# Optimization experiments

Measured on AMD Instinct MI355X. Metric: run time of the kernel, lower is better.

Reference implementation:

```python
import jax, jax.numpy as jnp
import numpy as np

# dims (match init_kwargs)
B, T, F = 2048, 252, 64      # batch, n_timestep, n_feature
C, L, K = 64, 4, 3           # channels, num levels, kernel_size
NOUT, NSEL = 500, 20         # n_output assets, n_select
LB, UB = 0.0, 0.1            # simplex box bounds
N_REBAL_ITERS = 16           # fixed bound on the water-filling loop (converges in a few iters)


def setup_inputs() -> dict:
    key = jax.random.key(0)
    ks = jax.random.split(key, 12)
    inp = {
        'x': jax.random.normal(ks[0], (B, T, F), dtype=jnp.float32),
        # TemporalBlock convs: init_weights() uses N(0, 0.01); weight_norm is a
        # reparametrization, so the effective conv weight is just a dense tensor.
        'conv1_w': 0.01 * jax.random.normal(ks[1], (L, C, C, K), dtype=jnp.float32),
        'conv1_b': 0.01 * jax.random.normal(ks[2], (L, C), dtype=jnp.float32),
        'conv2_w': 0.01 * jax.random.normal(ks[3], (L, C, C, K), dtype=jnp.float32),
        'conv2_b': 0.01 * jax.random.normal(ks[4], (L, C), dtype=jnp.float32),
        'proj_w': 0.05 * jax.random.normal(ks[5], (C, C), dtype=jnp.float32),
        'proj_b': 0.01 * jax.random.normal(ks[6], (C,), dtype=jnp.float32),
        'attn_w': 0.05 * jax.random.normal(ks[7], (NOUT, C), dtype=jnp.float32),
        'attn_b': 0.01 * jax.random.normal(ks[8], (NOUT,), dtype=jnp.float32),
        'fc_w': 0.05 * jax.random.normal(ks[9], (NOUT, C), dtype=jnp.float32),
        'fc_b': 0.01 * jax.random.normal(ks[10], (NOUT,), dtype=jnp.float32),
    }
    return inp


def _causal_conv(h, w, b, dil):
    # h: [B,C,T], w: [O,I,K]. torch pads both sides by (K-1)*dil then Chomp1d
    # removes the right pad -> equivalent to pure left (causal) padding.
    k = w.shape[-1]
    out = jax.lax.conv_general_dilated(
        h, w, window_strides=(1,), padding=[((k - 1) * dil, 0)],
        rhs_dilation=(dil,), dimension_numbers=('NCH', 'OIH', 'NCH'))
    return out + b[None, :, None]


def _rebalance(w, lb, ub, n_iters=N_REBAL_ITERS):
    # batched water-filling on the box-bounded simplex; mirrors the torch
    # do-while: redistribute clamped-off mass proportionally to non-capped weights.
    def step(old, wc):
        leftover = jnp.sum(old - wc)
        m = wc != ub
        nsum = jnp.sum(jnp.where(m, wc, 0.0))
        nsum = jnp.where(nsum == 0.0, 1.0, nsum)  # guard degenerate all-capped case
        return jnp.where(m, wc + leftover * wc / nsum, wc)

    cur = step(w, jnp.clip(w, lb, ub))           # first iteration (do-while)
    done0 = ~jnp.any(cur > ub)

    def body(carry, _):
        cur, done = carry
        nxt = step(cur, jnp.clip(cur, lb, ub))
        new = jnp.where(done, cur, nxt)
        return (new, done | ~jnp.any(new > ub)), None

    (res, _), _ = jax.lax.scan(body, (cur, done0), None, length=n_iters)
    return res


def reference(x, conv1_w, conv1_b, conv2_w, conv2_b,
              proj_w, proj_b, attn_w, attn_b, fc_w, fc_b):
    h = jnp.transpose(x, (0, 2, 1))  # [B,F,T]
    for i in range(L):  # fixed small loop over levels (structurally distinct dilations)
        d = 2 ** i
        o = jax.nn.relu(_causal_conv(h, conv1_w[i], conv1_b[i], d))
        o = jax.nn.relu(_causal_conv(o, conv2_w[i], conv2_b[i], d))
        h = jax.nn.relu(o + h)  # in==out channels -> identity residual
    pooled = jnp.max(h, axis=2)                       # MaxPool1d(T) + squeeze -> [B,C]
    z = jax.nn.relu(pooled @ proj_w.T + proj_b)       # proj (dropout=eval no-op)
    attn = jax.nn.sigmoid(z @ attn_w.T + attn_b)      # [B,NOUT]
    _, idx = jax.lax.top_k(attn, NSEL)
    mask = jnp.zeros_like(attn).at[jnp.arange(attn.shape[0])[:, None], idx].set(1.0)
    out = jax.nn.softmax(z @ fc_w.T + fc_b, axis=1) * mask
    out = out / (jnp.sum(out, axis=1, keepdims=True) + 1e-8)
    out = jax.vmap(lambda w: _rebalance(w, LB, UB))(out)
    return out
```

## Files before the change

kernel.cpp:

```cpp
#include <hip/hip_runtime.h>
#include <hip/hip_bf16.h>

#define T 252
#define NOUT 500
#define NSEL 20
#define UBV 0.1f

#define ROWS 272
#define PLANE_U (ROWS * 32)
#define LDS_BYTES (2 * PLANE_U * 4)

#define OFF_AWT    98304
#define OFF_FWT    130304
#define OFF_POOLED 162304

typedef short bf8 __attribute__((ext_vector_type(8)));
typedef float f32x4 __attribute__((ext_vector_type(4)));

static __device__ __forceinline__ unsigned short f2bf(float f) {
    unsigned u = __float_as_uint(f);
    return (unsigned short)((u + 0x7fffu + ((u >> 16) & 1u)) >> 16);
}
static __device__ __forceinline__ float bf2f(unsigned short h) {
    return __uint_as_float(((unsigned)h) << 16);
}
static __device__ __forceinline__ unsigned pk2bf(float a, float b) {
    __hip_bfloat162 h = __float22bfloat162_rn(float2{a, b});
    unsigned u; __builtin_memcpy(&u, &h, 4); return u;
}
static __device__ __forceinline__ float bf_lo_f(unsigned u) { return __uint_as_float(u << 16); }
static __device__ __forceinline__ float bf_hi_f(unsigned u) { return __uint_as_float(u & 0xffff0000u); }
static __device__ __forceinline__ int swz(int row, int chunk) {
    return row * 32 + ((chunk ^ (row & 7)) << 2);
}

__global__ __launch_bounds__(256) void prep_kernel(
    const float* __restrict__ w1, const float* __restrict__ w2,
    const float* __restrict__ aw, const float* __restrict__ fw,
    float* __restrict__ ws)
{
    int gid = blockIdx.x * 256 + threadIdx.x;
    if (gid < 24576) {
        int frag = gid >> 6, lane = gid & 63;
        int s   = frag & 1;
        int m   = (frag >> 1) & 3;
        int t3  = frag >> 3;
        int tap = t3 % 3;
        int q   = t3 / 3;
        int Kt  = q & 1;
        int lvl = (q >> 1) & 3;
        int buf = q >> 3;
        int c  = m * 16 + (lane & 15);
        int i0 = Kt * 32 + (lane >> 4) * 8;
        const float* W = (buf ? w2 : w1) + lvl * 12288 + c * 192;
        unsigned short v[8];
        for (int j = 0; j < 8; ++j) {
            float x = W[(i0 + j) * 3 + tap];
            unsigned short hi = f2bf(x);
            if (s == 0) v[j] = hi;
            else        v[j] = f2bf(x - bf2f(hi));
        }
        unsigned* dst = (unsigned*)ws + frag * 256 + lane * 4;
        for (int d = 0; d < 4; ++d)
            dst[d] = (unsigned)v[2 * d] | ((unsigned)v[2 * d + 1] << 16);
    }
    if (gid < 32000) {
        int a = gid >> 6, c = gid & 63;
        ws[OFF_AWT + c * 500 + a] = aw[gid];
        ws[OFF_FWT + c * 500 + a] = fw[gid];
    }
}

extern __shared__ unsigned short lds[];

#define MFMA(A, B, C) __builtin_amdgcn_mfma_f32_16x16x32_bf16((A), (B), (C), 0, 0, 0)

static __device__ __forceinline__ void conv_mm(
    const uint4* __restrict__ AF4,
    const unsigned* __restrict__ Lh, const unsigned* __restrict__ Ll,
    const float* __restrict__ bias,
    int cvlvl, int d, int Rb, int g, int g4, int lane,
    f32x4 acc[4][4])
{
    #pragma unroll
    for (int m = 0; m < 4; ++m) {
        float4 bv = *(const float4*)(bias + m * 16 + g4);
        #pragma unroll
        for (int nn = 0; nn < 4; ++nn)
            acc[m][nn] = (f32x4){bv.x, bv.y, bv.z, bv.w};
    }
    #pragma unroll
    for (int Kt = 0; Kt < 2; ++Kt) {
        #pragma unroll
        for (int tap = 0; tap < 3; ++tap) {
            const int fb = ((cvlvl * 2 + Kt) * 3 + tap) * 8;
            const uint4* af = AF4 + fb * 64 + lane;
            uint4 ta[4], tb[4];
            #pragma unroll
            for (int m = 0; m < 4; ++m) { ta[m] = af[m * 128]; tb[m] = af[m * 128 + 64]; }
            const int shift = (2 - tap) * d;
            const int row0  = Rb - shift;
            const int ui0   = row0 * 32 + ((((Kt << 2) + g) ^ (row0 & 7)) << 2);
            bf8 Bh[4], Bl[4];
            #pragma unroll
            for (int nn = 0; nn < 4; ++nn) {
                Bh[nn] = *(const bf8*)(Lh + ui0 + nn * 512);
                Bl[nn] = *(const bf8*)(Ll + ui0 + nn * 512);
            }
            #pragma unroll
            for (int m = 0; m < 4; ++m) {
                bf8 Ah = *(bf8*)&ta[m];
                bf8 Al = *(bf8*)&tb[m];
                #pragma unroll
                for (int nn = 0; nn < 4; ++nn) {
                    f32x4 a = acc[m][nn];
                    a = MFMA(Ah, Bh[nn], a);
                    a = MFMA(Ah, Bl[nn], a);
                    a = MFMA(Al, Bh[nn], a);
                    acc[m][nn] = a;
                }
            }
        }
    }
}

__global__ __launch_bounds__(256, 2) void conv_kernel(
    const float* __restrict__ x,
    const float* __restrict__ ws,
    const float* __restrict__ b1,
    const float* __restrict__ b2,
    float* __restrict__ pooled)
{
    const int b    = blockIdx.x;
    const int tid  = threadIdx.x;
    const int lane = tid & 63;
    const int wv   = tid >> 6;

    unsigned* Lh = (unsigned*)lds;
    unsigned* Ll = Lh + PLANE_U;

    for (int j = tid; j < 640; j += 256) {
        int r20 = j >> 5, col = j & 31;
        int r = (r20 < 16) ? r20 : (252 + r20);
        Lh[r * 32 + col] = 0u;
        Ll[r * 32 + col] = 0u;
    }
    const float4* xb = (const float4*)(x + (size_t)b * (T * 64));
    for (int v = tid; v < T * 16; v += 256) {
        float4 xv = xb[v];
        int t = v >> 4, f4 = v & 15;
        unsigned h01 = pk2bf(xv.x, xv.y);
        unsigned h23 = pk2bf(xv.z, xv.w);
        unsigned l01 = pk2bf(xv.x - bf_lo_f(h01), xv.y - bf_hi_f(h01));
        unsigned l23 = pk2bf(xv.z - bf_lo_f(h23), xv.w - bf_hi_f(h23));
        int row = 16 + t;
        int ui = swz(row, f4 >> 1) + ((f4 & 1) << 1);
        Lh[ui]     = h01;
        Lh[ui + 1] = h23;
        Ll[ui]     = l01;
        Ll[ui + 1] = l23;
    }

    const int g    = lane >> 4;
    const int g4   = g << 2;
    const int ln16 = lane & 15;
    const int Rb   = 16 + 64 * wv + ln16;

    float hr[4][4][4];
    #pragma unroll
    for (int m = 0; m < 4; ++m)
        #pragma unroll
        for (int nn = 0; nn < 4; ++nn) {
            int t = 64 * wv + 16 * nn + ln16;
            if (t < T) {
                float4 v = xb[t * 16 + m * 4 + g];
                hr[m][nn][0] = v.x; hr[m][nn][1] = v.y;
                hr[m][nn][2] = v.z; hr[m][nn][3] = v.w;
            } else {
                hr[m][nn][0] = 0.f; hr[m][nn][1] = 0.f;
                hr[m][nn][2] = 0.f; hr[m][nn][3] = 0.f;
            }
        }
    __syncthreads();

    const uint4* AF4 = (const uint4*)ws;

    int ue[4];
    #pragma unroll
    for (int m = 0; m < 4; ++m)
        ue[m] = Rb * 32 + (((2 * m + (g >> 1)) ^ (Rb & 7)) << 2) + ((g & 1) << 1);

    for (int lvl = 0; lvl < 4; ++lvl) {
        const int d = 1 << lvl;
        f32x4 acc[4][4];

        conv_mm(AF4, Lh, Ll, b1 + lvl * 64, 0 * 4 + lvl, d, Rb, g, g4, lane, acc);
        __syncthreads();
        #pragma unroll
        for (int m = 0; m < 4; ++m)
            #pragma unroll
            for (int nn = 0; nn < 4; ++nn) {
                float o0 = fmaxf(acc[m][nn][0], 0.f);
                float o1 = fmaxf(acc[m][nn][1], 0.f);
                float o2 = fmaxf(acc[m][nn][2], 0.f);
                float o3 = fmaxf(acc[m][nn][3], 0.f);
                uint2 wh, wl;
                wh.x = pk2bf(o0, o1);
                wh.y = pk2bf(o2, o3);
                wl.x = pk2bf(o0 - bf_lo_f(wh.x), o1 - bf_hi_f(wh.x));
                wl.y = pk2bf(o2 - bf_lo_f(wh.y), o3 - bf_hi_f(wh.y));
                int ui = ue[m] + nn * 512;
                *(uint2*)(Lh + ui) = wh;
                *(uint2*)(Ll + ui) = wl;
            }
        __syncthreads();

        conv_mm(AF4, Lh, Ll, b2 + lvl * 64, 1 * 4 + lvl, d, Rb, g, g4, lane, acc);
        #pragma unroll
        for (int m = 0; m < 4; ++m)
            #pragma unroll
            for (int nn = 0; nn < 4; ++nn)
                #pragma unroll
                for (int j = 0; j < 4; ++j)
                    hr[m][nn][j] = fmaxf(fmaxf(acc[m][nn][j], 0.f) + hr[m][nn][j], 0.f);

        if (lvl < 3) {
            __syncthreads();
            #pragma unroll
            for (int m = 0; m < 4; ++m)
                #pragma unroll
                for (int nn = 0; nn < 4; ++nn) {
                    float h0 = hr[m][nn][0], h1 = hr[m][nn][1];
                    float h2 = hr[m][nn][2], h3 = hr[m][nn][3];
                    uint2 wh, wl;
                    wh.x = pk2bf(h0, h1);
                    wh.y = pk2bf(h2, h3);
                    wl.x = pk2bf(h0 - bf_lo_f(wh.x), h1 - bf_hi_f(wh.x));
                    wl.y = pk2bf(h2 - bf_lo_f(wh.y), h3 - bf_hi_f(wh.y));
                    int ui = ue[m] + nn * 512;
                    *(uint2*)(Lh + ui) = wh;
                    *(uint2*)(Ll + ui) = wl;
                }
            __syncthreads();
        }
    }

    __syncthreads();
    {
        const bool t3ok = (64 * wv + 48 + ln16) < T;
        float pm[4][4];
        #pragma unroll
        for (int m = 0; m < 4; ++m)
            #pragma unroll
            for (int j = 0; j < 4; ++j) {
                float p = fmaxf(fmaxf(hr[m][0][j], hr[m][1][j]), hr[m][2][j]);
                if (t3ok) p = fmaxf(p, hr[m][3][j]);
                pm[m][j] = p;
            }
        #pragma unroll
        for (int off = 1; off < 16; off <<= 1)
            #pragma unroll
            for (int m = 0; m < 4; ++m)
                #pragma unroll
                for (int j = 0; j < 4; ++j)
                    pm[m][j] = fmaxf(pm[m][j], __shfl_xor(pm[m][j], off));
        float* fp = (float*)lds;
        if (ln16 == 0) {
            #pragma unroll
            for (int m = 0; m < 4; ++m)
                #pragma unroll
                for (int j = 0; j < 4; ++j)
                    fp[wv * 64 + m * 16 + g4 + j] = pm[m][j];
        }
        __syncthreads();
        if (tid < 64) {
            float mm = fmaxf(fmaxf(fp[tid], fp[tid + 64]),
                             fmaxf(fp[tid + 128], fp[tid + 192]));
            pooled[(size_t)b * 64 + tid] = mm;
        }
    }
}

__global__ __launch_bounds__(256) void head_kernel(
    const float* __restrict__ ws,
    const float* __restrict__ proj_w,
    const float* __restrict__ proj_b,
    const float* __restrict__ attn_b,
    const float* __restrict__ fc_b,
    float* __restrict__ out)
{
    const float* awT    = ws + OFF_AWT;
    const float* fwT    = ws + OFF_FWT;
    const float* pooled = ws + OFF_POOLED;

    __shared__ float z[64];
    __shared__ float att[512];
    __shared__ float pa[512];
    __shared__ int   msk[512];
    __shared__ float rs[4];

    const int b   = blockIdx.x;
    const int tid = threadIdx.x;
    const int wv  = tid >> 6, ln = tid & 63;

    {
        const int outc = tid >> 2, part = tid & 3;
        const float* pw = proj_w + outc * 64 + part * 16;
        const float* pl = pooled + (size_t)b * 64 + part * 16;
        float s = 0.f;
        #pragma unroll
        for (int c = 0; c < 16; ++c) s = fmaf(pw[c], pl[c], s);
        s += __shfl_xor(s, 1);
        s += __shfl_xor(s, 2);
        if (part == 0) z[outc] = fmaxf(s + proj_b[outc], 0.f);
    }
    __syncthreads();

    const int a0  = tid;
    const int a1  = tid + 256;
    const int a1e = (a1 < NOUT) ? a1 : (NOUT - 1);

    float l0 = attn_b[a0], l1 = attn_b[a1e];
    float f0 = fc_b[a0],   f1 = fc_b[a1e];
    #pragma unroll 8
    for (int c = 0; c < 64; ++c) {
        float zc = z[c];
        l0 = fmaf(zc, awT[c * 500 + a0],  l0);
        l1 = fmaf(zc, awT[c * 500 + a1e], l1);
        f0 = fmaf(zc, fwT[c * 500 + a0],  f0);
        f1 = fmaf(zc, fwT[c * 500 + a1e], f1);
    }
    float v0 = 1.f / (1.f + expf(-l0));
    float v1 = (a1 < NOUT) ? 1.f / (1.f + expf(-l1)) : 0.f;
    if (a1 >= NOUT) f1 = -1e30f;
    att[a0] = v0; att[a1] = v1;
    msk[a0] = 0;  msk[a1] = 0;
    __syncthreads();

    int selidx = 0;
    if (wv == 0) {
        float va[8];
        #pragma unroll
        for (int j = 0; j < 8; ++j) {
            int id = j * 64 + ln;
            va[j] = (id < NOUT) ? att[id] : 0.f;
        }
        for (int s = 0; s < NSEL; ++s) {
            float bv = va[0]; int bj = 0;
            #pragma unroll
            for (int j = 1; j < 8; ++j)
                if (va[j] > bv) { bv = va[j]; bj = j; }
            unsigned long long k =
                ((unsigned long long)__float_as_uint(bv) << 32)
                | (unsigned)(0xFFFFFFFFu - (unsigned)(bj * 64 + ln));
            for (int o = 32; o > 0; o >>= 1) {
                unsigned long long other = __shfl_xor(k, o);
                if (other > k) k = other;
            }
            int widx = (int)(0xFFFFFFFFu - (unsigned)(k & 0xFFFFFFFFu));
            if (ln == s) selidx = widx;
            if ((widx & 63) == ln) va[widx >> 6] = 0.f;
            if (ln == 0) msk[widx] = 1;
        }
    }
    __syncthreads();

    float mx = fmaxf(f0, f1);
    for (int o = 32; o > 0; o >>= 1) mx = fmaxf(mx, __shfl_xor(mx, o));
    if (ln == 0) rs[wv] = mx;
    __syncthreads();
    mx = fmaxf(fmaxf(rs[0], rs[1]), fmaxf(rs[2], rs[3]));
    __syncthreads();
    float e0 = expf(f0 - mx);
    float e1 = (a1 < NOUT) ? expf(f1 - mx) : 0.f;
    float sm = e0 + e1;
    for (int o = 32; o > 0; o >>= 1) sm += __shfl_xor(sm, o);
    if (ln == 0) rs[wv] = sm;
    __syncthreads();
    float Z = rs[0] + rs[1] + rs[2] + rs[3];

    float p0 = msk[a0] ? (e0 / Z) : 0.f;
    float p1 = (a1 < NOUT && msk[a1]) ? (e1 / Z) : 0.f;
    pa[a0] = p0; pa[a1] = p1;
    __syncthreads();

    if (wv == 0) {
        float w = (ln < NSEL) ? pa[selidx] : 0.f;
        float S = w;
        for (int o = 32; o > 0; o >>= 1) S += __shfl_xor(S, o);
        w = w / (S + 1e-8f);
        for (int it = 0; it < 17; ++it) {
            float wc = fminf(fmaxf(w, 0.f), UBV);
            float lo = w - wc;
            float ns = (wc != UBV) ? wc : 0.f;
            for (int o = 32; o > 0; o >>= 1) {
                lo += __shfl_xor(lo, o);
                ns += __shfl_xor(ns, o);
            }
            if (ns == 0.f) ns = 1.f;
            w = (wc != UBV) ? wc + lo * wc / ns : wc;
        }
        if (ln < NSEL) out[(size_t)b * NOUT + selidx] = w;
    }
    if (!msk[a0]) out[(size_t)b * NOUT + a0] = 0.f;
    if (a1 < NOUT && !msk[a1]) out[(size_t)b * NOUT + a1] = 0.f;
}

extern "C" void kernel_launch(void* const* d_in, const int* in_sizes, int n_in,
                              void* d_out, int out_size, void* d_ws, size_t ws_size,
                              hipStream_t stream)
{
    const float* x   = (const float*)d_in[0];
    const float* c1w = (const float*)d_in[1];
    const float* c1b = (const float*)d_in[2];
    const float* c2w = (const float*)d_in[3];
    const float* c2b = (const float*)d_in[4];
    const float* pw  = (const float*)d_in[5];
    const float* pb  = (const float*)d_in[6];
    const float* aw  = (const float*)d_in[7];
    const float* ab  = (const float*)d_in[8];
    const float* fw  = (const float*)d_in[9];
    const float* fb  = (const float*)d_in[10];

    float* ws  = (float*)d_ws;
    float* out = (float*)d_out;

    (void)hipFuncSetAttribute((const void*)conv_kernel,
                              hipFuncAttributeMaxDynamicSharedMemorySize,
                              LDS_BYTES);

    prep_kernel<<<128, 256, 0, stream>>>(c1w, c2w, aw, fw, ws);
    conv_kernel<<<2048, 256, LDS_BYTES, stream>>>(x, ws, c1b, c2b, ws + OFF_POOLED);
    head_kernel<<<2048, 256, 0, stream>>>(ws, pw, pb, ab, fb, out);
}
```

Before: 510.7 us.

## Use LDS-only barriers, prefetch first weight fragment, and stagger conv blocks

Replaces __syncthreads with a barrier that waits only on LDS counters, so outstanding global loads can stay in flight across barriers. The first weight fragment and bias for the next conv are prefetched before each barrier, overlapping those global loads with synchronisation. MFMA sections are wrapped in s_setprio, and every other group of 256 blocks sleeps briefly at start to stagger its phase against the co-resident block. The custom barrier depends on the compiler not needing vmcnt at those points, and the sleep adds latency if staggering does not help.

Result: slower. 545.8 us (+6.9%).

```diff
diff --git a/kernel.cpp b/kernel.cpp
--- a/kernel.cpp
+++ b/kernel.cpp
@@ -33,6 +33,12 @@
 static __device__ __forceinline__ int swz(int row, int chunk) {
     return row * 32 + ((chunk ^ (row & 7)) << 2);
 }
+
+#define BAR_LDS() do {                                        \
+    asm volatile("s_waitcnt lgkmcnt(0)" ::: "memory");        \
+    __builtin_amdgcn_s_barrier();                             \
+    asm volatile("" ::: "memory");                            \
+} while (0)
 
 __global__ __launch_bounds__(256) void prep_kernel(
     const float* __restrict__ w1, const float* __restrict__ w2,
@@ -75,16 +81,37 @@
 
 #define MFMA(A, B, C) __builtin_amdgcn_mfma_f32_16x16x32_bf16((A), (B), (C), 0, 0, 0)
 
+struct Frag0 {
+    uint4  ta[4], tb[4];
+    float4 bv[4];
+};
+
+static __device__ __forceinline__ Frag0 pf_frag0(
+    const uint4* __restrict__ AF4, int cvlvl, int lane,
+    const float* __restrict__ bias, int g4)
+{
+    Frag0 f;
+    const int fb = (cvlvl * 2 + 0) * 3 + 0;
+    const uint4* af = AF4 + fb * 8 * 64 + lane;
+    #pragma unroll
+    for (int m = 0; m < 4; ++m) {
+        f.ta[m] = af[m * 128];
+        f.tb[m] = af[m * 128 + 64];
+        f.bv[m] = *(const float4*)(bias + m * 16 + g4);
+    }
+    return f;
+}
+
 static __device__ __forceinline__ void conv_mm(
     const uint4* __restrict__ AF4,
     const unsigned* __restrict__ Lh, const unsigned* __restrict__ Ll,
-    const float* __restrict__ bias,
-    int cvlvl, int d, int Rb, int g, int g4, int lane,
+    const Frag0& f0,
+    int cvlvl, int d, int Rb, int g, int lane,
     f32x4 acc[4][4])
 {
     #pragma unroll
     for (int m = 0; m < 4; ++m) {
-        float4 bv = *(const float4*)(bias + m * 16 + g4);
+        float4 bv = f0.bv[m];
         #pragma unroll
         for (int nn = 0; nn < 4; ++nn)
             acc[m][nn] = (f32x4){bv.x, bv.y, bv.z, bv.w};
@@ -93,11 +120,16 @@
     for (int Kt = 0; Kt < 2; ++Kt) {
         #pragma unroll
         for (int tap = 0; tap < 3; ++tap) {
-            const int fb = ((cvlvl * 2 + Kt) * 3 + tap) * 8;
-            const uint4* af = AF4 + fb * 64 + lane;
             uint4 ta[4], tb[4];
-            #pragma unroll
-            for (int m = 0; m < 4; ++m) { ta[m] = af[m * 128]; tb[m] = af[m * 128 + 64]; }
+            if (Kt == 0 && tap == 0) {
+                #pragma unroll
+                for (int m = 0; m < 4; ++m) { ta[m] = f0.ta[m]; tb[m] = f0.tb[m]; }
+            } else {
+                const int fb = ((cvlvl * 2 + Kt) * 3 + tap) * 8;
+                const uint4* af = AF4 + fb * 64 + lane;
+                #pragma unroll
+                for (int m = 0; m < 4; ++m) { ta[m] = af[m * 128]; tb[m] = af[m * 128 + 64]; }
+            }
             const int shift = (2 - tap) * d;
             const int row0  = Rb - shift;
             const int ui0   = row0 * 32 + ((((Kt << 2) + g) ^ (row0 & 7)) << 2);
@@ -107,6 +139,7 @@
                 Bh[nn] = *(const bf8*)(Lh + ui0 + nn * 512);
                 Bl[nn] = *(const bf8*)(Ll + ui0 + nn * 512);
             }
+            __builtin_amdgcn_s_setprio(1);
             #pragma unroll
             for (int m = 0; m < 4; ++m) {
                 bf8 Ah = *(bf8*)&ta[m];
@@ -120,6 +153,7 @@
                     acc[m][nn] = a;
                 }
             }
+            __builtin_amdgcn_s_setprio(0);
         }
     }
 }
@@ -135,6 +169,8 @@
     const int tid  = threadIdx.x;
     const int lane = tid & 63;
     const int wv   = tid >> 6;
+
+    if ((blockIdx.x >> 8) & 1) __builtin_amdgcn_s_sleep(127);
 
     unsigned* Lh = (unsigned*)lds;
     unsigned* Ll = Lh + PLANE_U;
@@ -181,9 +217,11 @@
                 hr[m][nn][2] = 0.f; hr[m][nn][3] = 0.f;
             }
         }
-    __syncthreads();
 
     const uint4* AF4 = (const uint4*)ws;
+
+    Frag0 f0 = pf_frag0(AF4, 0, lane, b1, g4);
+    BAR_LDS();
 
     int ue[4];
     #pragma unroll
@@ -194,8 +232,8 @@
         const int d = 1 << lvl;
         f32x4 acc[4][4];
 
-        conv_mm(AF4, Lh, Ll, b1 + lvl * 64, 0 * 4 + lvl, d, Rb, g, g4, lane, acc);
-        __syncthreads();
+        conv_mm(AF4, Lh, Ll, f0, 0 * 4 + lvl, d, Rb, g, lane, acc);
+        BAR_LDS();
         #pragma unroll
         for (int m = 0; m < 4; ++m)
             #pragma unroll
@@ -213,9 +251,10 @@
                 *(uint2*)(Lh + ui) = wh;
                 *(uint2*)(Ll + ui) = wl;
             }
-        __syncthreads();
-
-        conv_mm(AF4, Lh, Ll, b2 + lvl * 64, 1 * 4 + lvl, d, Rb, g, g4, lane, acc);
+        f0 = pf_frag0(AF4, 1 * 4 + lvl, lane, b2 + lvl * 64, g4);
+        BAR_LDS();
+
+        conv_mm(AF4, Lh, Ll, f0, 1 * 4 + lvl, d, Rb, g, lane, acc);
         #pragma unroll
         for (int m = 0; m < 4; ++m)
             #pragma unroll
@@ -225,7 +264,7 @@
                     hr[m][nn][j] = fmaxf(fmaxf(acc[m][nn][j], 0.f) + hr[m][nn][j], 0.f);
 
         if (lvl < 3) {
-            __syncthreads();
+            BAR_LDS();
             #pragma unroll
             for (int m = 0; m < 4; ++m)
                 #pragma unroll
@@ -241,11 +280,12 @@
                     *(uint2*)(Lh + ui) = wh;
                     *(uint2*)(Ll + ui) = wl;
                 }
-            __syncthreads();
-        }
-    }
-
-    __syncthreads();
+            f0 = pf_frag0(AF4, 0 * 4 + (lvl + 1), lane, b1 + (lvl + 1) * 64, g4);
+            BAR_LDS();
+        }
+    }
+
+    BAR_LDS();
     {
         const bool t3ok = (64 * wv + 48 + ln16) < T;
         float pm[4][4];
@@ -272,7 +312,7 @@
                 for (int j = 0; j < 4; ++j)
                     fp[wv * 64 + m * 16 + g4 + j] = pm[m][j];
         }
-        __syncthreads();
+        BAR_LDS();
         if (tid < 64) {
             float mm = fmaxf(fmaxf(fp[tid], fp[tid + 64]),
                              fmaxf(fp[tid + 128], fp[tid + 192]));
```

## Ping-pong LDS activation buffers to drop barriers in conv levels

Applied to the files above, without the earlier changes.

Adds a second pair of hi/lo LDS planes so the intermediate conv1 output and the residual state go to different buffers. That removes two of the four block barriers per level. Remaining barriers become a raw lgkmcnt wait plus s_barrier. The extra planes double LDS use per block, so launch bounds drop to one block per CU. This gives up the latency hiding of a second resident block in exchange for fewer synchronisations.

Result: slower. 881.2 us (+72.5%).

```diff
diff --git a/kernel.cpp b/kernel.cpp
--- a/kernel.cpp
+++ b/kernel.cpp
@@ -8,7 +8,7 @@
 
 #define ROWS 272
 #define PLANE_U (ROWS * 32)
-#define LDS_BYTES (2 * PLANE_U * 4)
+#define LDS_BYTES (4 * PLANE_U * 4)
 
 #define OFF_AWT    98304
 #define OFF_FWT    130304
@@ -33,6 +33,12 @@
 static __device__ __forceinline__ int swz(int row, int chunk) {
     return row * 32 + ((chunk ^ (row & 7)) << 2);
 }
+
+#define BAR_LDS() do {                                        \
+    asm volatile("s_waitcnt lgkmcnt(0)" ::: "memory");        \
+    __builtin_amdgcn_s_barrier();                             \
+    asm volatile("" ::: "memory");                            \
+} while (0)
 
 __global__ __launch_bounds__(256) void prep_kernel(
     const float* __restrict__ w1, const float* __restrict__ w2,
@@ -124,7 +130,7 @@
     }
 }
 
-__global__ __launch_bounds__(256, 2) void conv_kernel(
+__global__ __launch_bounds__(256, 1) void conv_kernel(
     const float* __restrict__ x,
     const float* __restrict__ ws,
     const float* __restrict__ b1,
@@ -136,14 +142,18 @@
     const int lane = tid & 63;
     const int wv   = tid >> 6;
 
-    unsigned* Lh = (unsigned*)lds;
-    unsigned* Ll = Lh + PLANE_U;
+    unsigned* LAh = (unsigned*)lds;
+    unsigned* LAl = LAh + PLANE_U;
+    unsigned* LBh = LAh + 2 * PLANE_U;
+    unsigned* LBl = LAh + 3 * PLANE_U;
 
     for (int j = tid; j < 640; j += 256) {
         int r20 = j >> 5, col = j & 31;
         int r = (r20 < 16) ? r20 : (252 + r20);
-        Lh[r * 32 + col] = 0u;
-        Ll[r * 32 + col] = 0u;
+        LAh[r * 32 + col] = 0u;
+        LAl[r * 32 + col] = 0u;
+        LBh[r * 32 + col] = 0u;
+        LBl[r * 32 + col] = 0u;
     }
     const float4* xb = (const float4*)(x + (size_t)b * (T * 64));
     for (int v = tid; v < T * 16; v += 256) {
@@ -155,10 +165,10 @@
         unsigned l23 = pk2bf(xv.z - bf_lo_f(h23), xv.w - bf_hi_f(h23));
         int row = 16 + t;
         int ui = swz(row, f4 >> 1) + ((f4 & 1) << 1);
-        Lh[ui]     = h01;
-        Lh[ui + 1] = h23;
-        Ll[ui]     = l01;
-        Ll[ui + 1] = l23;
+        LAh[ui]     = h01;
+        LAh[ui + 1] = h23;
+        LAl[ui]     = l01;
+        LAl[ui + 1] = l23;
     }
 
     const int g    = lane >> 4;
@@ -181,7 +191,7 @@
                 hr[m][nn][2] = 0.f; hr[m][nn][3] = 0.f;
             }
         }
-    __syncthreads();
+    BAR_LDS();
 
     const uint4* AF4 = (const uint4*)ws;
 
@@ -194,8 +204,7 @@
         const int d = 1 << lvl;
         f32x4 acc[4][4];
 
-        conv_mm(AF4, Lh, Ll, b1 + lvl * 64, 0 * 4 + lvl, d, Rb, g, g4, lane, acc);
-        __syncthreads();
+        conv_mm(AF4, LAh, LAl, b1 + lvl * 64, 0 * 4 + lvl, d, Rb, g, g4, lane, acc);
         #pragma unroll
         for (int m = 0; m < 4; ++m)
             #pragma unroll
@@ -210,12 +219,12 @@
                 wl.x = pk2bf(o0 - bf_lo_f(wh.x), o1 - bf_hi_f(wh.x));
                 wl.y = pk2bf(o2 - bf_lo_f(wh.y), o3 - bf_hi_f(wh.y));
                 int ui = ue[m] + nn * 512;
-                *(uint2*)(Lh + ui) = wh;
-                *(uint2*)(Ll + ui) = wl;
-            }
-        __syncthreads();
-
-        conv_mm(AF4, Lh, Ll, b2 + lvl * 64, 1 * 4 + lvl, d, Rb, g, g4, lane, acc);
+                *(uint2*)(LBh + ui) = wh;
+                *(uint2*)(LBl + ui) = wl;
+            }
+        BAR_LDS();
+
+        conv_mm(AF4, LBh, LBl, b2 + lvl * 64, 1 * 4 + lvl, d, Rb, g, g4, lane, acc);
         #pragma unroll
         for (int m = 0; m < 4; ++m)
             #pragma unroll
@@ -225,7 +234,6 @@
                     hr[m][nn][j] = fmaxf(fmaxf(acc[m][nn][j], 0.f) + hr[m][nn][j], 0.f);
 
         if (lvl < 3) {
-            __syncthreads();
             #pragma unroll
             for (int m = 0; m < 4; ++m)
                 #pragma unroll
@@ -238,14 +246,13 @@
                     wl.x = pk2bf(h0 - bf_lo_f(wh.x), h1 - bf_hi_f(wh.x));
                     wl.y = pk2bf(h2 - bf_lo_f(wh.y), h3 - bf_hi_f(wh.y));
                     int ui = ue[m] + nn * 512;
-                    *(uint2*)(Lh + ui) = wh;
-                    *(uint2*)(Ll + ui) = wl;
+                    *(uint2*)(LAh + ui) = wh;
+                    *(uint2*)(LAl + ui) = wl;
                 }
-            __syncthreads();
-        }
-    }
-
-    __syncthreads();
+            BAR_LDS();
+        }
+    }
+
     {
         const bool t3ok = (64 * wv + 48 + ln16) < T;
         float pm[4][4];
@@ -272,7 +279,7 @@
                 for (int j = 0; j < 4; ++j)
                     fp[wv * 64 + m * 16 + g4 + j] = pm[m][j];
         }
-        __syncthreads();
+        BAR_LDS();
         if (tid < 64) {
             float mm = fmaxf(fmaxf(fp[tid], fp[tid + 64]),
                              fmaxf(fp[tid + 128], fp[tid + 192]));
```

## Switch conv MFMA tiles from 16x16x32 to 32x32x16 bf16

Applied to the files above, without the earlier changes.

Recasts the per-wave conv GEMM to use 32x32x16 bf16 MFMAs with 2x2 tiles of 16-element accumulators instead of 4x4 tiles of 16x16x32 ops. The weight fragment packing in prep, the LDS read and write addressing, the residual register layout and the max-pool reduction are all remapped to the new accumulator layout. The aim is fewer MFMA issues and fewer LDS fragment loads per tap, since each B fragment is reused across a larger tile. The pooling shuffle reduction now spans 32 lanes instead of 16.

New measurement: 539.2 us. 5.6% more time.

```diff
diff --git a/kernel.cpp b/kernel.cpp
--- a/kernel.cpp
+++ b/kernel.cpp
@@ -15,7 +15,7 @@
 #define OFF_POOLED 162304
 
 typedef short bf8 __attribute__((ext_vector_type(8)));
-typedef float f32x4 __attribute__((ext_vector_type(4)));
+typedef float f32x16 __attribute__((ext_vector_type(16)));
 
 static __device__ __forceinline__ unsigned short f2bf(float f) {
     unsigned u = __float_as_uint(f);
@@ -42,16 +42,16 @@
     int gid = blockIdx.x * 256 + threadIdx.x;
     if (gid < 24576) {
         int frag = gid >> 6, lane = gid & 63;
-        int s   = frag & 1;
-        int m   = (frag >> 1) & 3;
-        int t3  = frag >> 3;
-        int tap = t3 % 3;
-        int q   = t3 / 3;
-        int Kt  = q & 1;
-        int lvl = (q >> 1) & 3;
-        int buf = q >> 3;
-        int c  = m * 16 + (lane & 15);
-        int i0 = Kt * 32 + (lane >> 4) * 8;
+        int s    = frag & 1;
+        int m    = (frag >> 1) & 1;
+        int Kt   = (frag >> 2) & 3;
+        int rest = frag >> 4;
+        int tap  = rest % 3;
+        int cl   = rest / 3;
+        int lvl  = cl & 3;
+        int buf  = cl >> 2;
+        int c  = m * 32 + (lane & 31);
+        int i0 = Kt * 16 + (lane >> 5) * 8;
         const float* W = (buf ? w2 : w1) + lvl * 12288 + c * 192;
         unsigned short v[8];
         for (int j = 0; j < 8; ++j) {
@@ -73,50 +73,55 @@
 
 extern __shared__ unsigned short lds[];
 
-#define MFMA(A, B, C) __builtin_amdgcn_mfma_f32_16x16x32_bf16((A), (B), (C), 0, 0, 0)
-
-static __device__ __forceinline__ void conv_mm(
+#define MFMA32(A, B, C) __builtin_amdgcn_mfma_f32_32x32x16_bf16((A), (B), (C), 0, 0, 0)
+
+static __device__ __forceinline__ void conv_mm32(
     const uint4* __restrict__ AF4,
     const unsigned* __restrict__ Lh, const unsigned* __restrict__ Ll,
     const float* __restrict__ bias,
-    int cvlvl, int d, int Rb, int g, int g4, int lane,
-    f32x4 acc[4][4])
+    int cvlvl, int d, int Rb, int half, int lane,
+    f32x16 acc[2][2])
 {
     #pragma unroll
-    for (int m = 0; m < 4; ++m) {
-        float4 bv = *(const float4*)(bias + m * 16 + g4);
-        #pragma unroll
-        for (int nn = 0; nn < 4; ++nn)
-            acc[m][nn] = (f32x4){bv.x, bv.y, bv.z, bv.w};
-    }
+    for (int m = 0; m < 2; ++m)
+        #pragma unroll
+        for (int q = 0; q < 4; ++q) {
+            float4 bv = *(const float4*)(bias + m * 32 + q * 8 + half * 4);
+            #pragma unroll
+            for (int nn = 0; nn < 2; ++nn) {
+                acc[m][nn][4 * q + 0] = bv.x;
+                acc[m][nn][4 * q + 1] = bv.y;
+                acc[m][nn][4 * q + 2] = bv.z;
+                acc[m][nn][4 * q + 3] = bv.w;
+            }
+        }
     #pragma unroll
-    for (int Kt = 0; Kt < 2; ++Kt) {
+    for (int Kt = 0; Kt < 4; ++Kt) {
         #pragma unroll
         for (int tap = 0; tap < 3; ++tap) {
-            const int fb = ((cvlvl * 2 + Kt) * 3 + tap) * 8;
+            const int fb = (((cvlvl * 3 + tap) * 4 + Kt) << 2);
             const uint4* af = AF4 + fb * 64 + lane;
-            uint4 ta[4], tb[4];
-            #pragma unroll
-            for (int m = 0; m < 4; ++m) { ta[m] = af[m * 128]; tb[m] = af[m * 128 + 64]; }
+            uint4 ta[2], tb[2];
+            ta[0] = af[0];   tb[0] = af[64];
+            ta[1] = af[128]; tb[1] = af[192];
             const int shift = (2 - tap) * d;
             const int row0  = Rb - shift;
-            const int ui0   = row0 * 32 + ((((Kt << 2) + g) ^ (row0 & 7)) << 2);
-            bf8 Bh[4], Bl[4];
-            #pragma unroll
-            for (int nn = 0; nn < 4; ++nn) {
-                Bh[nn] = *(const bf8*)(Lh + ui0 + nn * 512);
-                Bl[nn] = *(const bf8*)(Ll + ui0 + nn * 512);
-            }
-            #pragma unroll
-            for (int m = 0; m < 4; ++m) {
+            const int ui0   = row0 * 32 + ((((Kt << 1) + half) ^ (row0 & 7)) << 2);
+            bf8 Bh[2], Bl[2];
+            Bh[0] = *(const bf8*)(Lh + ui0);
+            Bh[1] = *(const bf8*)(Lh + ui0 + 1024);
+            Bl[0] = *(const bf8*)(Ll + ui0);
+            Bl[1] = *(const bf8*)(Ll + ui0 + 1024);
+            #pragma unroll
+            for (int m = 0; m < 2; ++m) {
                 bf8 Ah = *(bf8*)&ta[m];
                 bf8 Al = *(bf8*)&tb[m];
                 #pragma unroll
-                for (int nn = 0; nn < 4; ++nn) {
-                    f32x4 a = acc[m][nn];
-                    a = MFMA(Ah, Bh[nn], a);
-                    a = MFMA(Ah, Bl[nn], a);
-                    a = MFMA(Al, Bh[nn], a);
+                for (int nn = 0; nn < 2; ++nn) {
+                    f32x16 a = acc[m][nn];
+                    a = MFMA32(Ah, Bh[nn], a);
+                    a = MFMA32(Ah, Bl[nn], a);
+                    a = MFMA32(Al, Bh[nn], a);
                     acc[m][nn] = a;
                 }
             }
@@ -161,116 +166,128 @@
         Ll[ui + 1] = l23;
     }
 
-    const int g    = lane >> 4;
-    const int g4   = g << 2;
-    const int ln16 = lane & 15;
-    const int Rb   = 16 + 64 * wv + ln16;
-
-    float hr[4][4][4];
+    const int l31  = lane & 31;
+    const int half = lane >> 5;
+    const int Rb   = 16 + 64 * wv + l31;
+
+    float hr[2][2][16];
     #pragma unroll
-    for (int m = 0; m < 4; ++m)
-        #pragma unroll
-        for (int nn = 0; nn < 4; ++nn) {
-            int t = 64 * wv + 16 * nn + ln16;
-            if (t < T) {
-                float4 v = xb[t * 16 + m * 4 + g];
-                hr[m][nn][0] = v.x; hr[m][nn][1] = v.y;
-                hr[m][nn][2] = v.z; hr[m][nn][3] = v.w;
-            } else {
-                hr[m][nn][0] = 0.f; hr[m][nn][1] = 0.f;
-                hr[m][nn][2] = 0.f; hr[m][nn][3] = 0.f;
+    for (int m = 0; m < 2; ++m)
+        #pragma unroll
+        for (int nn = 0; nn < 2; ++nn) {
+            int t = 64 * wv + 32 * nn + l31;
+            #pragma unroll
+            for (int q = 0; q < 4; ++q) {
+                if (t < T) {
+                    float4 v = xb[t * 16 + m * 8 + 2 * q + half];
+                    hr[m][nn][4 * q + 0] = v.x; hr[m][nn][4 * q + 1] = v.y;
+                    hr[m][nn][4 * q + 2] = v.z; hr[m][nn][4 * q + 3] = v.w;
+                } else {
+                    hr[m][nn][4 * q + 0] = 0.f; hr[m][nn][4 * q + 1] = 0.f;
+                    hr[m][nn][4 * q + 2] = 0.f; hr[m][nn][4 * q + 3] = 0.f;
+                }
             }
         }
     __syncthreads();
 
     const uint4* AF4 = (const uint4*)ws;
 
-    int ue[4];
+    int ue[2][4];
     #pragma unroll
-    for (int m = 0; m < 4; ++m)
-        ue[m] = Rb * 32 + (((2 * m + (g >> 1)) ^ (Rb & 7)) << 2) + ((g & 1) << 1);
+    for (int m = 0; m < 2; ++m)
+        #pragma unroll
+        for (int q = 0; q < 4; ++q)
+            ue[m][q] = Rb * 32 + ((((m << 2) + q) ^ (Rb & 7)) << 2) + (half << 1);
 
     for (int lvl = 0; lvl < 4; ++lvl) {
         const int d = 1 << lvl;
-        f32x4 acc[4][4];
-
-        conv_mm(AF4, Lh, Ll, b1 + lvl * 64, 0 * 4 + lvl, d, Rb, g, g4, lane, acc);
+        f32x16 acc[2][2];
+
+        conv_mm32(AF4, Lh, Ll, b1 + lvl * 64, 0 * 4 + lvl, d, Rb, half, lane, acc);
         __syncthreads();
         #pragma unroll
-        for (int m = 0; m < 4; ++m)
-            #pragma unroll
-            for (int nn = 0; nn < 4; ++nn) {
-                float o0 = fmaxf(acc[m][nn][0], 0.f);
-                float o1 = fmaxf(acc[m][nn][1], 0.f);
-                float o2 = fmaxf(acc[m][nn][2], 0.f);
-                float o3 = fmaxf(acc[m][nn][3], 0.f);
-                uint2 wh, wl;
-                wh.x = pk2bf(o0, o1);
-                wh.y = pk2bf(o2, o3);
-                wl.x = pk2bf(o0 - bf_lo_f(wh.x), o1 - bf_hi_f(wh.x));
-                wl.y = pk2bf(o2 - bf_lo_f(wh.y), o3 - bf_hi_f(wh.y));
-                int ui = ue[m] + nn * 512;
-                *(uint2*)(Lh + ui) = wh;
-                *(uint2*)(Ll + ui) = wl;
-            }
-        __syncthreads();
-
-        conv_mm(AF4, Lh, Ll, b2 + lvl * 64, 1 * 4 + lvl, d, Rb, g, g4, lane, acc);
-        #pragma unroll
-        for (int m = 0; m < 4; ++m)
-            #pragma unroll
-            for (int nn = 0; nn < 4; ++nn)
-                #pragma unroll
-                for (int j = 0; j < 4; ++j)
-                    hr[m][nn][j] = fmaxf(fmaxf(acc[m][nn][j], 0.f) + hr[m][nn][j], 0.f);
-
-        if (lvl < 3) {
-            __syncthreads();
-            #pragma unroll
-            for (int m = 0; m < 4; ++m)
-                #pragma unroll
-                for (int nn = 0; nn < 4; ++nn) {
-                    float h0 = hr[m][nn][0], h1 = hr[m][nn][1];
-                    float h2 = hr[m][nn][2], h3 = hr[m][nn][3];
+        for (int m = 0; m < 2; ++m)
+            #pragma unroll
+            for (int nn = 0; nn < 2; ++nn)
+                #pragma unroll
+                for (int q = 0; q < 4; ++q) {
+                    float o0 = fmaxf(acc[m][nn][4 * q + 0], 0.f);
+                    float o1 = fmaxf(acc[m][nn][4 * q + 1], 0.f);
+                    float o2 = fmaxf(acc[m][nn][4 * q + 2], 0.f);
+                    float o3 = fmaxf(acc[m][nn][4 * q + 3], 0.f);
                     uint2 wh, wl;
-                    wh.x = pk2bf(h0, h1);
-                    wh.y = pk2bf(h2, h3);
-                    wl.x = pk2bf(h0 - bf_lo_f(wh.x), h1 - bf_hi_f(wh.x));
-                    wl.y = pk2bf(h2 - bf_lo_f(wh.y), h3 - bf_hi_f(wh.y));
-                    int ui = ue[m] + nn * 512;
+                    wh.x = pk2bf(o0, o1);
+                    wh.y = pk2bf(o2, o3);
+                    wl.x = pk2bf(o0 - bf_lo_f(wh.x), o1 - bf_hi_f(wh.x));
+                    wl.y = pk2bf(o2 - bf_lo_f(wh.y), o3 - bf_hi_f(wh.y));
+                    int ui = ue[m][q] + nn * 1024;
                     *(uint2*)(Lh + ui) = wh;
                     *(uint2*)(Ll + ui) = wl;
                 }
+        __syncthreads();
+
+        conv_mm32(AF4, Lh, Ll, b2 + lvl * 64, 1 * 4 + lvl, d, Rb, half, lane, acc);
+        #pragma unroll
+        for (int m = 0; m < 2; ++m)
+            #pragma unroll
+            for (int nn = 0; nn < 2; ++nn)
+                #pragma unroll
+                for (int r = 0; r < 16; ++r)
+                    hr[m][nn][r] = fmaxf(fmaxf(acc[m][nn][r], 0.f) + hr[m][nn][r], 0.f);
+
+        if (lvl < 3) {
             __syncthreads();
+            #pragma unroll
+            for (int m = 0; m < 2; ++m)
+                #pragma unroll
+                for (int nn = 0; nn < 2; ++nn)
+                    #pragma unroll
+                    for (int q = 0; q < 4; ++q) {
+                        float h0 = hr[m][nn][4 * q + 0], h1 = hr[m][nn][4 * q + 1];
+                        float h2 = hr[m][nn][4 * q + 2], h3 = hr[m][nn][4 * q + 3];
+                        uint2 wh, wl;
+                        wh.x = pk2bf(h0, h1);
+                        wh.y = pk2bf(h2, h3);
+                        wl.x = pk2bf(h0 - bf_lo_f(wh.x), h1 - bf_hi_f(wh.x));
+                        wl.y = pk2bf(h2 - bf_lo_f(wh.y), h3 - bf_hi_f(wh.y));
+                        int ui = ue[m][q] + nn * 1024;
+                        *(uint2*)(Lh + ui) = wh;
+                        *(uint2*)(Ll + ui) = wl;
+                    }
+            __syncthreads();
         }
     }
 
     __syncthreads();
     {
-        const bool t3ok = (64 * wv + 48 + ln16) < T;
-        float pm[4][4];
-        #pragma unroll
-        for (int m = 0; m < 4; ++m)
-            #pragma unroll
-            for (int j = 0; j < 4; ++j) {
-                float p = fmaxf(fmaxf(hr[m][0][j], hr[m][1][j]), hr[m][2][j]);
-                if (t3ok) p = fmaxf(p, hr[m][3][j]);
-                pm[m][j] = p;
-            }
-        #pragma unroll
-        for (int off = 1; off < 16; off <<= 1)
-            #pragma unroll
-            for (int m = 0; m < 4; ++m)
-                #pragma unroll
-                for (int j = 0; j < 4; ++j)
-                    pm[m][j] = fmaxf(pm[m][j], __shfl_xor(pm[m][j], off));
+        const bool ok1 = (64 * wv + 32 + l31) < T;
+        float pm[2][16];
+        #pragma unroll
+        for (int m = 0; m < 2; ++m)
+            #pragma unroll
+            for (int r = 0; r < 16; ++r) {
+                float p = hr[m][0][r];
+                if (ok1) p = fmaxf(p, hr[m][1][r]);
+                pm[m][r] = p;
+            }
+        #pragma unroll
+        for (int off = 1; off < 32; off <<= 1)
+            #pragma unroll
+            for (int m = 0; m < 2; ++m)
+                #pragma unroll
+                for (int r = 0; r < 16; ++r)
+                    pm[m][r] = fmaxf(pm[m][r], __shfl_xor(pm[m][r], off));
         float* fp = (float*)lds;
-        if (ln16 == 0) {
-            #pragma unroll
-            for (int m = 0; m < 4; ++m)
-                #pragma unroll
-                for (int j = 0; j < 4; ++j)
-                    fp[wv * 64 + m * 16 + g4 + j] = pm[m][j];
+        if (l31 == 0) {
+            #pragma unroll
+            for (int m = 0; m < 2; ++m)
+                #pragma unroll
+                for (int q = 0; q < 4; ++q) {
+                    float4 v;
+                    v.x = pm[m][4 * q + 0]; v.y = pm[m][4 * q + 1];
+                    v.z = pm[m][4 * q + 2]; v.w = pm[m][4 * q + 3];
+                    *(float4*)(fp + wv * 64 + m * 32 + q * 8 + half * 4) = v;
+                }
         }
         __syncthreads();
         if (tid < 64) {
```
